# Kernel tuning notes

Measured on AMD Instinct MI355X. Metric: run time of the kernel, lower is better.

Reference implementation:

```python
import jax, jax.numpy as jnp
import numpy as np
import math

N_HEADS = 16


def _rope(t, cos, sin):
    # t: [B, S, H, d_k] with d_k paired as (even, odd) -> complex multiply by cos+i*sin
    B, S, H, dk = t.shape
    t = t.reshape(B, S, H, dk // 2, 2)
    t0, t1 = t[..., 0], t[..., 1]
    c = cos[None, :S, None, :]
    s = sin[None, :S, None, :]
    out = jnp.stack([t0 * c - t1 * s, t0 * s + t1 * c], axis=-1)
    return out.reshape(B, S, H, dk)


def setup_inputs() -> dict:
    key = jax.random.key(0)
    ks = jax.random.split(key, 6)
    B, S, D = 2, 2048, 2048
    dk = D // N_HEADS  # 128
    x = jax.random.normal(ks[0], (B, S, D), dtype=jnp.float32)
    # standard RoPE angle table
    inv_freq = 1.0 / (10000.0 ** (np.arange(0, dk, 2, dtype=np.float32) / dk))  # [dk/2]
    t = np.arange(S, dtype=np.float32)
    ang = np.outer(t, inv_freq)  # [S, dk/2]
    freqs_cos = jnp.asarray(np.cos(ang), dtype=jnp.float32)
    freqs_sin = jnp.asarray(np.sin(ang), dtype=jnp.float32)
    # additive causal mask [1,1,S,S]
    causal = jnp.tril(jnp.ones((S, S), dtype=bool))
    mask = jnp.where(causal, 0.0, -1e9).astype(jnp.float32)[None, None]
    wscale = 1.0 / math.sqrt(D)
    Wq = jax.random.normal(ks[1], (D, D), dtype=jnp.float32) * wscale
    Wk = jax.random.normal(ks[2], (D, D), dtype=jnp.float32) * wscale
    Wv = jax.random.normal(ks[3], (D, D), dtype=jnp.float32) * wscale
    Wo = jax.random.normal(ks[4], (D, D), dtype=jnp.float32) * wscale
    return {"x": x, "freqs_cos": freqs_cos, "freqs_sin": freqs_sin, "mask": mask,
            "Wq": Wq, "Wk": Wk, "Wv": Wv, "Wo": Wo}


def reference(x, freqs_cos, freqs_sin, mask, Wq, Wk, Wv, Wo):
    B, S, D = x.shape
    H = N_HEADS
    dk = D // H
    scale = math.sqrt(dk)
    # nn.Linear(w) applies x @ w.T
    Q = (x @ Wq.T).reshape(B, S, H, dk)
    K = (x @ Wk.T).reshape(B, S, H, dk)
    V = (x @ Wv.T).reshape(B, S, H, dk)
    Q = _rope(Q, freqs_cos, freqs_sin)
    K = _rope(K, freqs_cos, freqs_sin)
    new_kv_cache = (K, V)  # kv_cache=None path: cache is just current K, V
    # [B, H, S, dk]
    Qh = Q.transpose(0, 2, 1, 3)
    Kh = K.transpose(0, 2, 1, 3)
    Vh = V.transpose(0, 2, 1, 3)
    scores = jnp.einsum('bhqd,bhkd->bhqk', Qh, Kh) / scale + mask
    attn = jax.nn.softmax(scores, axis=-1)  # dropout=0 (eval)
    ctx = jnp.einsum('bhqk,bhkd->bhqd', attn, Vh)
    ctx = ctx.transpose(0, 2, 1, 3).reshape(B, S, D)
    output = ctx @ Wo.T
    return output, new_kv_cache[0], new_kv_cache[1]
```

## Files before the change

kernel.cpp:

```cpp
#include <hip/hip_runtime.h>
#include <hip/hip_bf16.h>

#define SEQ   2048
#define DIM   2048
#define NH    16
#define DKH   128
#define BATCH 2
#define MROWS (BATCH * SEQ)
#define NQT   (SEQ / 64)

using bf16 = __hip_bfloat16;
typedef __attribute__((ext_vector_type(8))) short short8;
typedef __attribute__((ext_vector_type(4))) short short4v;
typedef __attribute__((ext_vector_type(4))) float floatx4;

union BfBits { bf16 h; short s; };

__device__ __forceinline__ void gl_lds16(const bf16* g, bf16* l) {
  __builtin_amdgcn_global_load_lds(
      (__attribute__((address_space(1))) void*)(g),
      (__attribute__((address_space(3))) void*)(l), 16, 0, 0);
}

__global__ __launch_bounds__(256) void cast5_kernel(const float* __restrict__ x,
                                                    const float* __restrict__ wq,
                                                    const float* __restrict__ wk,
                                                    const float* __restrict__ wv,
                                                    const float* __restrict__ wo,
                                                    bf16* __restrict__ dst,
                                                    int nX4, int nW4, int nTot) {
  int i = blockIdx.x * 256 + threadIdx.x;
  if (i >= nTot) return;
  const float* src;
  int off;
  int j = i - nX4;
  if (j < 0) { src = x; off = i; }
  else {
    int wsel = j >> 20;
    off = j & (nW4 - 1);
    src = (wsel == 0) ? wq : (wsel == 1) ? wk : (wsel == 2) ? wv : wo;
  }
  float4 v = reinterpret_cast<const float4*>(src)[off];
  __hip_bfloat162 h01, h23;
  h01.x = __float2bfloat16(v.x); h01.y = __float2bfloat16(v.y);
  h23.x = __float2bfloat16(v.z); h23.y = __float2bfloat16(v.w);
  reinterpret_cast<__hip_bfloat162*>(dst)[i * 2 + 0] = h01;
  reinterpret_cast<__hip_bfloat162*>(dst)[i * 2 + 1] = h23;
}

__global__ __launch_bounds__(256) void gemm_qkv(const bf16* __restrict__ A,
                                                const bf16* __restrict__ Bw,
                                                bf16* __restrict__ Qraw,
                                                float* __restrict__ Kout,
                                                float* __restrict__ Vout) {
  __shared__ bf16 As[128 * 32];
  __shared__ bf16 Bs[128 * 32];
  const int t = threadIdx.x;
  const int m0 = blockIdx.y * 128;
  const int n0 = blockIdx.x * 128;
  const int w = t >> 6, lane = t & 63;
  const int wm = (w >> 1) * 64, wn = (w & 1) * 64;
  const int lr = lane & 15, quad = lane >> 4;

  const int c0 = w * 2;
  const int r0 = lane >> 2;
  const int kc = (lane & 3) * 8;

  floatx4 acc[4][4];
#pragma unroll
  for (int i = 0; i < 4; ++i)
#pragma unroll
    for (int j = 0; j < 4; ++j)
      acc[i][j] = (floatx4){0.f, 0.f, 0.f, 0.f};

  for (int k0 = 0; k0 < DIM; k0 += 32) {
    gl_lds16(A + (size_t)(m0 + c0 * 16 + r0) * DIM + k0 + kc,       As + c0 * 512);
    gl_lds16(A + (size_t)(m0 + (c0 + 1) * 16 + r0) * DIM + k0 + kc, As + (c0 + 1) * 512);
    gl_lds16(Bw + (size_t)(n0 + c0 * 16 + r0) * DIM + k0 + kc,       Bs + c0 * 512);
    gl_lds16(Bw + (size_t)(n0 + (c0 + 1) * 16 + r0) * DIM + k0 + kc, Bs + (c0 + 1) * 512);
    __syncthreads();

    short8 af[4], bfr[4];
#pragma unroll
    for (int i = 0; i < 4; ++i)
      af[i] = *reinterpret_cast<const short8*>(As + (wm + i * 16 + lr) * 32 + quad * 8);
#pragma unroll
    for (int j = 0; j < 4; ++j)
      bfr[j] = *reinterpret_cast<const short8*>(Bs + (wn + j * 16 + lr) * 32 + quad * 8);
#pragma unroll
    for (int i = 0; i < 4; ++i)
#pragma unroll
      for (int j = 0; j < 4; ++j)
        acc[i][j] = __builtin_amdgcn_mfma_f32_16x16x32_bf16(af[i], bfr[j], acc[i][j], 0, 0, 0);
    __syncthreads();
  }

  const int region = n0 >> 11;
#pragma unroll
  for (int i = 0; i < 4; ++i)
#pragma unroll
    for (int j = 0; j < 4; ++j) {
      int mrow = m0 + wm + i * 16 + quad * 4;
      int lcol = (n0 & 2047) + wn + j * 16 + lr;
#pragma unroll
      for (int rr = 0; rr < 4; ++rr) {
        size_t idx = (size_t)(mrow + rr) * DIM + lcol;
        if (region == 0)      Qraw[idx] = __float2bfloat16(acc[i][j][rr]);
        else if (region == 1) Kout[idx] = acc[i][j][rr];
        else                  Vout[idx] = acc[i][j][rr];
      }
    }
}

template <typename CT>
__global__ __launch_bounds__(256) void gemm_bt(const bf16* __restrict__ A,
                                               const bf16* __restrict__ Bw,
                                               CT* __restrict__ C,
                                               int M, int N, int K) {
  __shared__ bf16 As[128 * 32];
  __shared__ bf16 Bs[128 * 32];
  const int t = threadIdx.x;
  const int m0 = blockIdx.y * 128;
  const int n0 = blockIdx.x * 128;
  const int w = t >> 6, lane = t & 63;
  const int wm = (w >> 1) * 64, wn = (w & 1) * 64;
  const int lr = lane & 15, quad = lane >> 4;

  const int c0 = w * 2;
  const int r0 = lane >> 2;
  const int kc = (lane & 3) * 8;

  floatx4 acc[4][4];
#pragma unroll
  for (int i = 0; i < 4; ++i)
#pragma unroll
    for (int j = 0; j < 4; ++j)
      acc[i][j] = (floatx4){0.f, 0.f, 0.f, 0.f};

  for (int k0 = 0; k0 < K; k0 += 32) {
    gl_lds16(A + (size_t)(m0 + c0 * 16 + r0) * K + k0 + kc,       As + c0 * 512);
    gl_lds16(A + (size_t)(m0 + (c0 + 1) * 16 + r0) * K + k0 + kc, As + (c0 + 1) * 512);
    gl_lds16(Bw + (size_t)(n0 + c0 * 16 + r0) * K + k0 + kc,       Bs + c0 * 512);
    gl_lds16(Bw + (size_t)(n0 + (c0 + 1) * 16 + r0) * K + k0 + kc, Bs + (c0 + 1) * 512);
    __syncthreads();

    short8 af[4], bfr[4];
#pragma unroll
    for (int i = 0; i < 4; ++i)
      af[i] = *reinterpret_cast<const short8*>(As + (wm + i * 16 + lr) * 32 + quad * 8);
#pragma unroll
    for (int j = 0; j < 4; ++j)
      bfr[j] = *reinterpret_cast<const short8*>(Bs + (wn + j * 16 + lr) * 32 + quad * 8);
#pragma unroll
    for (int i = 0; i < 4; ++i)
#pragma unroll
      for (int j = 0; j < 4; ++j)
        acc[i][j] = __builtin_amdgcn_mfma_f32_16x16x32_bf16(af[i], bfr[j], acc[i][j], 0, 0, 0);
    __syncthreads();
  }

#pragma unroll
  for (int i = 0; i < 4; ++i)
#pragma unroll
    for (int j = 0; j < 4; ++j) {
      int mrow = m0 + wm + i * 16 + quad * 4;
      int ncol = n0 + wn + j * 16 + lr;
#pragma unroll
      for (int rr = 0; rr < 4; ++rr) {
        if constexpr (__is_same(CT, float))
          C[(size_t)(mrow + rr) * N + ncol] = acc[i][j][rr];
        else
          C[(size_t)(mrow + rr) * N + ncol] = __float2bfloat16(acc[i][j][rr]);
      }
    }
}

__global__ __launch_bounds__(256) void rope_q(const bf16* __restrict__ Qraw,
                                              const float* __restrict__ cosT,
                                              const float* __restrict__ sinT,
                                              bf16* __restrict__ Qb) {
  int g = blockIdx.x * 256 + threadIdx.x;
  int p = g & 63;
  int r = g >> 6;
  int h = r & 15;
  int s = (r >> 4) & (SEQ - 1);
  int b = r >> 15;
  __hip_bfloat162 v = reinterpret_cast<const __hip_bfloat162*>(Qraw)[g];
  float x0 = __bfloat162float(v.x), x1 = __bfloat162float(v.y);
  float c = cosT[s * 64 + p], sn = sinT[s * 64 + p];
  __hip_bfloat162 o;
  o.x = __float2bfloat16(x0 * c - x1 * sn);
  o.y = __float2bfloat16(x0 * sn + x1 * c);
  reinterpret_cast<__hip_bfloat162*>(Qb)[((size_t)(b * NH + h) * SEQ + s) * 64 + p] = o;
}

__global__ __launch_bounds__(256) void rope_k(float* __restrict__ Kf,
                                              const float* __restrict__ cosT,
                                              const float* __restrict__ sinT,
                                              bf16* __restrict__ Kb) {
  int g = blockIdx.x * 256 + threadIdx.x;
  int p = g & 63;
  int r = g >> 6;
  int h = r & 15;
  int s = (r >> 4) & (SEQ - 1);
  int b = r >> 15;
  float2 v = reinterpret_cast<const float2*>(Kf)[g];
  float c = cosT[s * 64 + p], sn = sinT[s * 64 + p];
  float o0 = v.x * c - v.y * sn;
  float o1 = v.x * sn + v.y * c;
  reinterpret_cast<float2*>(Kf)[g] = make_float2(o0, o1);
  __hip_bfloat162 ob;
  ob.x = __float2bfloat16(o0);
  ob.y = __float2bfloat16(o1);
  reinterpret_cast<__hip_bfloat162*>(Kb)[((size_t)(b * NH + h) * SEQ + s) * 64 + p] = ob;
}

__global__ __launch_bounds__(256) void vt_kernel(const float* __restrict__ V,
                                                 bf16* __restrict__ Vt) {
  __shared__ float tile[32][33];
  const int s0 = blockIdx.x * 32;
  const int d0 = blockIdx.y * 32;
  const int bh = blockIdx.z;
  const int b = bh >> 4, h = bh & 15;
  const int t = threadIdx.x;
  const int row = t >> 3, c4 = (t & 7) * 4;

  float4 v = *reinterpret_cast<const float4*>(
      V + (size_t)(b * SEQ + s0 + row) * DIM + h * DKH + d0 + c4);
  tile[row][c4 + 0] = v.x; tile[row][c4 + 1] = v.y;
  tile[row][c4 + 2] = v.z; tile[row][c4 + 3] = v.w;
  __syncthreads();

  short4v ov;
#pragma unroll
  for (int i = 0; i < 4; ++i) {
    BfBits u; u.h = __float2bfloat16(tile[c4 + i][row]);
    ov[i] = u.s;
  }
  *reinterpret_cast<short4v*>(Vt + ((size_t)(b * NH + h) * DKH + d0 + row) * SEQ + s0 + c4) = ov;
}

__global__ __launch_bounds__(256) void attn_mfma(const bf16* __restrict__ Qb,
                                                 const bf16* __restrict__ Kb,
                                                 const bf16* __restrict__ Vt,
                                                 bf16* __restrict__ ctx) {
  const int bx = blockIdx.x;
  const int h = blockIdx.y;
  const int b = blockIdx.z;
  const int t = threadIdx.x;
  const int w = t >> 6, lane = t & 63;
  const int lr = lane & 15, quad = lane >> 4;

  __shared__ short Ks[64 * 136];
  __shared__ short Vs[128 * 72];
  __shared__ short Ps[4 * 16 * 72];

  const float scale2 = 0.08838834764831845f * 1.44269504f;
  const float THR = 11.5413f;
  const size_t headQK = (size_t)(b * NH + h) * SEQ * DKH;

  for (int pass = 0; pass < 2; ++pass) {
    const int qt = pass ? bx : (NQT - 1 - bx);

    short8 qa[4];
    {
      const short* qbase = (const short*)Qb + headQK + (size_t)(qt * 64 + w * 16 + lr) * DKH;
#pragma unroll
      for (int kk = 0; kk < 4; ++kk)
        qa[kk] = *reinterpret_cast<const short8*>(qbase + kk * 32 + quad * 8);
    }

    floatx4 o[8];
#pragma unroll
    for (int n = 0; n < 8; ++n) o[n] = (floatx4){0.f, 0.f, 0.f, 0.f};
    float m[4] = {-1e30f, -1e30f, -1e30f, -1e30f};
    float l[4] = {0.f, 0.f, 0.f, 0.f};

    for (int kt = 0; kt <= qt; ++kt) {
      {
        const short* kbase = (const short*)Kb + headQK + (size_t)(kt * 64) * DKH;
#pragma unroll
        for (int u = 0; u < 4; ++u) {
          int c = t + 256 * u;
          *reinterpret_cast<int4*>(Ks + (c >> 4) * 136 + (c & 15) * 8) =
              *reinterpret_cast<const int4*>(kbase + c * 8);
        }
        const short* vbase = (const short*)Vt + (size_t)(b * NH + h) * DKH * SEQ + kt * 64;
#pragma unroll
        for (int u = 0; u < 4; ++u) {
          int c = t + 256 * u;
          *reinterpret_cast<int4*>(Vs + (c >> 3) * 72 + (c & 7) * 8) =
              *reinterpret_cast<const int4*>(vbase + (size_t)(c >> 3) * SEQ + (c & 7) * 8);
        }
      }
      __syncthreads();

      floatx4 sj[4];
#pragma unroll
      for (int j = 0; j < 4; ++j) sj[j] = (floatx4){0.f, 0.f, 0.f, 0.f};
#pragma unroll
      for (int j = 0; j < 4; ++j)
#pragma unroll
        for (int kk = 0; kk < 4; ++kk) {
          short8 kb = *reinterpret_cast<const short8*>(Ks + (j * 16 + lr) * 136 + kk * 32 + quad * 8);
          sj[j] = __builtin_amdgcn_mfma_f32_16x16x32_bf16(qa[kk], kb, sj[j], 0, 0, 0);
        }

      float sc[4][4];
#pragma unroll
      for (int j = 0; j < 4; ++j)
#pragma unroll
        for (int r = 0; r < 4; ++r) sc[j][r] = sj[j][r] * scale2;
      if (kt == qt) {
#pragma unroll
        for (int j = 0; j < 4; ++j) {
          int col = kt * 64 + j * 16 + lr;
#pragma unroll
          for (int r = 0; r < 4; ++r) {
            int rowg = qt * 64 + w * 16 + quad * 4 + r;
            if (col > rowg) sc[j][r] = -1e9f;
          }
        }
      }

#pragma unroll
      for (int r = 0; r < 4; ++r) {
        float mx = fmaxf(fmaxf(sc[0][r], sc[1][r]), fmaxf(sc[2][r], sc[3][r]));
        mx = fmaxf(mx, __shfl_xor(mx, 1, 16));
        mx = fmaxf(mx, __shfl_xor(mx, 2, 16));
        mx = fmaxf(mx, __shfl_xor(mx, 4, 16));
        mx = fmaxf(mx, __shfl_xor(mx, 8, 16));
        if (!__all(mx - m[r] <= THR)) {
          float mnew = fmaxf(m[r], mx);
          float alpha = __builtin_amdgcn_exp2f(m[r] - mnew);
          l[r] *= alpha;
#pragma unroll
          for (int n = 0; n < 8; ++n) o[n][r] *= alpha;
          m[r] = mnew;
        }
        float rs = 0.f;
#pragma unroll
        for (int j = 0; j < 4; ++j) {
          float p = __builtin_amdgcn_exp2f(sc[j][r] - m[r]);
          rs += p;
          BfBits u; u.h = __float2bfloat16(p);
          Ps[(w * 16 + quad * 4 + r) * 72 + j * 16 + lr] = u.s;
        }
        rs += __shfl_xor(rs, 1, 16);
        rs += __shfl_xor(rs, 2, 16);
        rs += __shfl_xor(rs, 4, 16);
        rs += __shfl_xor(rs, 8, 16);
        l[r] += rs;
      }

      short8 pa0 = *reinterpret_cast<const short8*>(Ps + (w * 16 + lr) * 72 + quad * 8);
      short8 pa1 = *reinterpret_cast<const short8*>(Ps + (w * 16 + lr) * 72 + 32 + quad * 8);
#pragma unroll
      for (int n = 0; n < 8; ++n) {
        short8 vb0 = *reinterpret_cast<const short8*>(Vs + (n * 16 + lr) * 72 + quad * 8);
        short8 vb1 = *reinterpret_cast<const short8*>(Vs + (n * 16 + lr) * 72 + 32 + quad * 8);
        o[n] = __builtin_amdgcn_mfma_f32_16x16x32_bf16(pa0, vb0, o[n], 0, 0, 0);
        o[n] = __builtin_amdgcn_mfma_f32_16x16x32_bf16(pa1, vb1, o[n], 0, 0, 0);
      }
      __syncthreads();
    }

    float inv[4];
#pragma unroll
    for (int r = 0; r < 4; ++r) inv[r] = 1.0f / l[r];
#pragma unroll
    for (int r = 0; r < 4; ++r) {
      size_t mrow = (size_t)b * SEQ + qt * 64 + w * 16 + quad * 4 + r;
      bf16* dst = ctx + mrow * DIM + h * DKH;
#pragma unroll
      for (int n = 0; n < 8; ++n)
        dst[n * 16 + lr] = __float2bfloat16(o[n][r] * inv[r]);
    }
  }
}

extern "C" void kernel_launch(void* const* d_in, const int* in_sizes, int n_in,
                              void* d_out, int out_size, void* d_ws, size_t ws_size,
                              hipStream_t stream) {
  const float* x = (const float*)d_in[0];
  const float* fcos = (const float*)d_in[1];
  const float* fsin = (const float*)d_in[2];
  const float* Wq = (const float*)d_in[4];
  const float* Wk = (const float*)d_in[5];
  const float* Wv = (const float*)d_in[6];
  const float* Wo = (const float*)d_in[7];

  float* out = (float*)d_out;
  float* Kout = out + (size_t)MROWS * DIM;
  float* Vout = Kout + (size_t)MROWS * DIM;

  const size_t MD = (size_t)MROWS * DIM;
  const size_t DD = (size_t)DIM * DIM;
  bf16* xb   = (bf16*)d_ws;
  bf16* Wqb  = xb + MD;
  bf16* Wkb  = Wqb + DD;
  bf16* Wvb  = Wkb + DD;
  bf16* Wob  = Wvb + DD;
  bf16* Qraw = Wob + DD;
  bf16* Qb   = Qraw + MD;
  bf16* Kb   = Qb + MD;
  bf16* Vt   = Kb + MD;
  bf16* ctxb = Qraw;

  const int nXD4 = MROWS * DIM / 4;
  const int nWD4 = DIM * DIM / 4;
  const int nTot = nXD4 + 4 * nWD4;
  cast5_kernel<<<nTot / 256, 256, 0, stream>>>(x, Wq, Wk, Wv, Wo, xb, nXD4, nWD4, nTot);

  dim3 gq(3 * DIM / 128, MROWS / 128);
  gemm_qkv<<<gq, 256, 0, stream>>>(xb, Wqb, Qraw, Kout, Vout);

  const int npairs = MROWS * DIM / 2;
  rope_q<<<npairs / 256, 256, 0, stream>>>(Qraw, fcos, fsin, Qb);
  rope_k<<<npairs / 256, 256, 0, stream>>>(Kout, fcos, fsin, Kb);

  dim3 gv(SEQ / 32, DKH / 32, BATCH * NH);
  vt_kernel<<<gv, 256, 0, stream>>>(Vout, Vt);

  dim3 ga(NQT / 2, NH, BATCH);
  attn_mfma<<<ga, 256, 0, stream>>>(Qb, Kb, Vt, ctxb);

  dim3 gg(DIM / 128, MROWS / 128);
  gemm_bt<float><<<gg, 256, 0, stream>>>(ctxb, Wob, out, MROWS, DIM, DIM);
}
```

Before: 520.2 us.

## Replace projection GEMMs with 256x128 double-buffered swizzled-LDS MFMA kernel

Replaces the 128x128 single-buffered QKV and output-projection GEMMs with one templated 256x128 tile kernel using 512 threads, BK=64, an XOR-swizzled LDS layout and a two-stage prefetch pipeline controlled by explicit vmcnt waits and raw barriers. The aim is to hide global-to-LDS load latency behind MFMA work, cut LDS bank conflicts, and raise per-block data reuse. It also raises MFMA priority with setprio. In exchange it uses more LDS and registers per block, and the hand-written waitcnt and barrier sequencing is fragile.

```diff
diff --git a/kernel.cpp b/kernel.cpp
--- a/kernel.cpp
+++ b/kernel.cpp
@@ -21,6 +21,11 @@
       (__attribute__((address_space(1))) void*)(g),
       (__attribute__((address_space(3))) void*)(l), 16, 0, 0);
 }
+
+#define S_BAR  __builtin_amdgcn_s_barrier()
+#define VMCNT6 do { asm volatile("s_waitcnt vmcnt(6)" ::: "memory"); __builtin_amdgcn_sched_barrier(0); } while (0)
+#define VMCNT0 do { asm volatile("s_waitcnt vmcnt(0)" ::: "memory"); __builtin_amdgcn_sched_barrier(0); } while (0)
+#define LGKM0  do { asm volatile("s_waitcnt lgkmcnt(0)" ::: "memory"); __builtin_amdgcn_sched_barrier(0); } while (0)
 
 __global__ __launch_bounds__(256) void cast5_kernel(const float* __restrict__ x,
                                                     const float* __restrict__ wq,
@@ -48,129 +53,120 @@
   reinterpret_cast<__hip_bfloat162*>(dst)[i * 2 + 1] = h23;
 }
 
-__global__ __launch_bounds__(256) void gemm_qkv(const bf16* __restrict__ A,
-                                                const bf16* __restrict__ Bw,
-                                                bf16* __restrict__ Qraw,
-                                                float* __restrict__ Kout,
-                                                float* __restrict__ Vout) {
-  __shared__ bf16 As[128 * 32];
-  __shared__ bf16 Bs[128 * 32];
+template <int ROWS>
+__device__ __forceinline__ void stage_swz(const bf16* __restrict__ G, bf16* lds,
+                                          int row0, int k0, int w, int l) {
+  const int rr = w * 8 + (l >> 3);
+  const int cc = ((l & 7) * 8) ^ ((l >> 3) * 8);
+#pragma unroll
+  for (int u = 0; u < ROWS / 64; ++u)
+    gl_lds16(G + (size_t)(row0 + u * 64 + rr) * DIM + k0 + cc,
+             lds + (u * 64 + w * 8) * 64);
+}
+
+template <int MODE>
+__global__ __launch_bounds__(512, 2) void gemm256(const bf16* __restrict__ A,
+                                                  const bf16* __restrict__ Bw,
+                                                  bf16* __restrict__ Qraw,
+                                                  float* __restrict__ Kout,
+                                                  float* __restrict__ Vout) {
+  __shared__ bf16 smem[2 * 256 * 64 + 2 * 128 * 64];
+  bf16* LA = smem;
+  bf16* LB = smem + 2 * 256 * 64;
+
   const int t = threadIdx.x;
-  const int m0 = blockIdx.y * 128;
-  const int n0 = blockIdx.x * 128;
-  const int w = t >> 6, lane = t & 63;
-  const int wm = (w >> 1) * 64, wn = (w & 1) * 64;
-  const int lr = lane & 15, quad = lane >> 4;
-
-  const int c0 = w * 2;
-  const int r0 = lane >> 2;
-  const int kc = (lane & 3) * 8;
-
-  floatx4 acc[4][4];
-#pragma unroll
-  for (int i = 0; i < 4; ++i)
-#pragma unroll
-    for (int j = 0; j < 4; ++j)
-      acc[i][j] = (floatx4){0.f, 0.f, 0.f, 0.f};
-
-  for (int k0 = 0; k0 < DIM; k0 += 32) {
-    gl_lds16(A + (size_t)(m0 + c0 * 16 + r0) * DIM + k0 + kc,       As + c0 * 512);
-    gl_lds16(A + (size_t)(m0 + (c0 + 1) * 16 + r0) * DIM + k0 + kc, As + (c0 + 1) * 512);
-    gl_lds16(Bw + (size_t)(n0 + c0 * 16 + r0) * DIM + k0 + kc,       Bs + c0 * 512);
-    gl_lds16(Bw + (size_t)(n0 + (c0 + 1) * 16 + r0) * DIM + k0 + kc, Bs + (c0 + 1) * 512);
-    __syncthreads();
-
-    short8 af[4], bfr[4];
-#pragma unroll
-    for (int i = 0; i < 4; ++i)
-      af[i] = *reinterpret_cast<const short8*>(As + (wm + i * 16 + lr) * 32 + quad * 8);
-#pragma unroll
-    for (int j = 0; j < 4; ++j)
-      bfr[j] = *reinterpret_cast<const short8*>(Bs + (wn + j * 16 + lr) * 32 + quad * 8);
-#pragma unroll
-    for (int i = 0; i < 4; ++i)
-#pragma unroll
-      for (int j = 0; j < 4; ++j)
-        acc[i][j] = __builtin_amdgcn_mfma_f32_16x16x32_bf16(af[i], bfr[j], acc[i][j], 0, 0, 0);
-    __syncthreads();
+  const int w = t >> 6, l = t & 63;
+  const int lr = l & 15, quad = l >> 4;
+  const int wr = w >> 2;
+  const int wc = w & 3;
+  const int m0 = blockIdx.y * 256;
+  const int n0g = blockIdx.x * 128;
+
+  const int cb = ((quad * 8) ^ ((lr & 7) * 8));
+
+  floatx4 acc[8][2];
+#pragma unroll
+  for (int mi = 0; mi < 8; ++mi)
+#pragma unroll
+    for (int nj = 0; nj < 2; ++nj) acc[mi][nj] = (floatx4){0.f, 0.f, 0.f, 0.f};
+
+  const int NT = DIM / 64;
+
+  stage_swz<256>(A, LA, m0, 0, w, l);
+  stage_swz<128>(Bw, LB, n0g, 0, w, l);
+  stage_swz<256>(A, LA + 256 * 64, m0, 64, w, l);
+  stage_swz<128>(Bw, LB + 128 * 64, n0g, 64, w, l);
+  VMCNT6;
+  S_BAR;
+
+  int cur = 0;
+  for (int kt = 0; kt < NT; ++kt) {
+    const bf16* la = LA + cur * (256 * 64);
+    const bf16* lb = LB + cur * (128 * 64);
+
+    short8 bfr[2][2];
+#pragma unroll
+    for (int nj = 0; nj < 2; ++nj) {
+      int rb = (wc * 32 + nj * 16 + lr) * 64;
+      bfr[nj][0] = *reinterpret_cast<const short8*>(lb + rb + cb);
+      bfr[nj][1] = *reinterpret_cast<const short8*>(lb + rb + (cb ^ 32));
+    }
+
+#pragma unroll
+    for (int qp = 0; qp < 4; ++qp) {
+      short8 af[4][2];
+#pragma unroll
+      for (int i = 0; i < 4; ++i) {
+        int ra = (wr * 128 + (qp * 4 + i) * 16 + lr) * 64;
+        af[i][0] = *reinterpret_cast<const short8*>(la + ra + cb);
+        af[i][1] = *reinterpret_cast<const short8*>(la + ra + (cb ^ 32));
+      }
+      LGKM0;
+      __builtin_amdgcn_s_setprio(1);
+#pragma unroll
+      for (int i = 0; i < 4; ++i)
+#pragma unroll
+        for (int nj = 0; nj < 2; ++nj) {
+          acc[qp * 4 + i][nj] = __builtin_amdgcn_mfma_f32_16x16x32_bf16(
+              af[i][0], bfr[nj][0], acc[qp * 4 + i][nj], 0, 0, 0);
+          acc[qp * 4 + i][nj] = __builtin_amdgcn_mfma_f32_16x16x32_bf16(
+              af[i][1], bfr[nj][1], acc[qp * 4 + i][nj], 0, 0, 0);
+        }
+      __builtin_amdgcn_s_setprio(0);
+    }
+
+    S_BAR;
+    if (kt + 2 < NT) {
+      stage_swz<256>(A, LA + cur * (256 * 64), m0, (kt + 2) * 64, w, l);
+      stage_swz<128>(Bw, LB + cur * (128 * 64), n0g, (kt + 2) * 64, w, l);
+      VMCNT6;
+    } else {
+      VMCNT0;
+    }
+    S_BAR;
+    cur ^= 1;
   }
 
-  const int region = n0 >> 11;
-#pragma unroll
-  for (int i = 0; i < 4; ++i)
-#pragma unroll
-    for (int j = 0; j < 4; ++j) {
-      int mrow = m0 + wm + i * 16 + quad * 4;
-      int lcol = (n0 & 2047) + wn + j * 16 + lr;
-#pragma unroll
-      for (int rr = 0; rr < 4; ++rr) {
-        size_t idx = (size_t)(mrow + rr) * DIM + lcol;
-        if (region == 0)      Qraw[idx] = __float2bfloat16(acc[i][j][rr]);
-        else if (region == 1) Kout[idx] = acc[i][j][rr];
-        else                  Vout[idx] = acc[i][j][rr];
-      }
-    }
-}
-
-template <typename CT>
-__global__ __launch_bounds__(256) void gemm_bt(const bf16* __restrict__ A,
-                                               const bf16* __restrict__ Bw,
-                                               CT* __restrict__ C,
-                                               int M, int N, int K) {
-  __shared__ bf16 As[128 * 32];
-  __shared__ bf16 Bs[128 * 32];
-  const int t = threadIdx.x;
-  const int m0 = blockIdx.y * 128;
-  const int n0 = blockIdx.x * 128;
-  const int w = t >> 6, lane = t & 63;
-  const int wm = (w >> 1) * 64, wn = (w & 1) * 64;
-  const int lr = lane & 15, quad = lane >> 4;
-
-  const int c0 = w * 2;
-  const int r0 = lane >> 2;
-  const int kc = (lane & 3) * 8;
-
-  floatx4 acc[4][4];
-#pragma unroll
-  for (int i = 0; i < 4; ++i)
-#pragma unroll
-    for (int j = 0; j < 4; ++j)
-      acc[i][j] = (floatx4){0.f, 0.f, 0.f, 0.f};
-
-  for (int k0 = 0; k0 < K; k0 += 32) {
-    gl_lds16(A + (size_t)(m0 + c0 * 16 + r0) * K + k0 + kc,       As + c0 * 512);
-    gl_lds16(A + (size_t)(m0 + (c0 + 1) * 16 + r0) * K + k0 + kc, As + (c0 + 1) * 512);
-    gl_lds16(Bw + (size_t)(n0 + c0 * 16 + r0) * K + k0 + kc,       Bs + c0 * 512);
-    gl_lds16(Bw + (size_t)(n0 + (c0 + 1) * 16 + r0) * K + k0 + kc, Bs + (c0 + 1) * 512);
-    __syncthreads();
-
-    short8 af[4], bfr[4];
-#pragma unroll
-    for (int i = 0; i < 4; ++i)
-      af[i] = *reinterpret_cast<const short8*>(As + (wm + i * 16 + lr) * 32 + quad * 8);
-#pragma unroll
-    for (int j = 0; j < 4; ++j)
-      bfr[j] = *reinterpret_cast<const short8*>(Bs + (wn + j * 16 + lr) * 32 + quad * 8);
-#pragma unroll
-    for (int i = 0; i < 4; ++i)
-#pragma unroll
-      for (int j = 0; j < 4; ++j)
-        acc[i][j] = __builtin_amdgcn_mfma_f32_16x16x32_bf16(af[i], bfr[j], acc[i][j], 0, 0, 0);
-    __syncthreads();
-  }
-
-#pragma unroll
-  for (int i = 0; i < 4; ++i)
-#pragma unroll
-    for (int j = 0; j < 4; ++j) {
-      int mrow = m0 + wm + i * 16 + quad * 4;
-      int ncol = n0 + wn + j * 16 + lr;
-#pragma unroll
-      for (int rr = 0; rr < 4; ++rr) {
-        if constexpr (__is_same(CT, float))
-          C[(size_t)(mrow + rr) * N + ncol] = acc[i][j][rr];
-        else
-          C[(size_t)(mrow + rr) * N + ncol] = __float2bfloat16(acc[i][j][rr]);
+#pragma unroll
+  for (int mi = 0; mi < 8; ++mi)
+#pragma unroll
+    for (int nj = 0; nj < 2; ++nj) {
+      int rg = m0 + wr * 128 + mi * 16 + quad * 4;
+      if constexpr (MODE == 0) {
+        const int region = n0g >> 11;
+        int lcol = (n0g & 2047) + wc * 32 + nj * 16 + lr;
+#pragma unroll
+        for (int rr2 = 0; rr2 < 4; ++rr2) {
+          size_t idx = (size_t)(rg + rr2) * DIM + lcol;
+          if (region == 0)      Qraw[idx] = __float2bfloat16(acc[mi][nj][rr2]);
+          else if (region == 1) Kout[idx] = acc[mi][nj][rr2];
+          else                  Vout[idx] = acc[mi][nj][rr2];
+        }
+      } else {
+        int lcol = n0g + wc * 32 + nj * 16 + lr;
+#pragma unroll
+        for (int rr2 = 0; rr2 < 4; ++rr2)
+          Kout[(size_t)(rg + rr2) * DIM + lcol] = acc[mi][nj][rr2];
       }
     }
 }
@@ -412,8 +408,8 @@
   const int nTot = nXD4 + 4 * nWD4;
   cast5_kernel<<<nTot / 256, 256, 0, stream>>>(x, Wq, Wk, Wv, Wo, xb, nXD4, nWD4, nTot);
 
-  dim3 gq(3 * DIM / 128, MROWS / 128);
-  gemm_qkv<<<gq, 256, 0, stream>>>(xb, Wqb, Qraw, Kout, Vout);
+  dim3 gq(3 * DIM / 128, MROWS / 256);
+  gemm256<0><<<gq, 512, 0, stream>>>(xb, Wqb, Qraw, Kout, Vout);
 
   const int npairs = MROWS * DIM / 2;
   rope_q<<<npairs / 256, 256, 0, stream>>>(Qraw, fcos, fsin, Qb);
@@ -425,6 +421,6 @@
   dim3 ga(NQT / 2, NH, BATCH);
   attn_mfma<<<ga, 256, 0, stream>>>(Qb, Kb, Vt, ctxb);
 
-  dim3 gg(DIM / 128, MROWS / 128);
-  gemm_bt<float><<<gg, 256, 0, stream>>>(ctxb, Wob, out, MROWS, DIM, DIM);
-}
+  dim3 go(DIM / 128, MROWS / 256);
+  gemm256<1><<<go, 512, 0, stream>>>(ctxb, Wob, (bf16*)nullptr, out, (float*)nullptr);
+}
```

After: 476.6 us. 1.09x faster.
